# Kernel optimization log

Measured on AMD Instinct MI355X. Metric: run time of the kernel, lower is better.

## Reference

```python
import jax, jax.numpy as jnp
import numpy as np

N = 100000      # nodes
E = 1600000     # edges
IN_C = 128
HID = 64
OUT_C = 40
LAYERS = 8
ALPHA = 0.1
THETA = 0.5
BN_EPS = 1e-5


def setup_inputs() -> dict:
    key = jax.random.key(0)
    ks = jax.random.split(key, 8)
    x = jax.random.normal(ks[0], (N, IN_C), jnp.float32)
    edge_index = jax.random.randint(ks[1], (2, E), 0, N, dtype=jnp.int64)
    W0 = jax.random.normal(ks[2], (IN_C, HID), jnp.float32) / np.sqrt(IN_C).astype(np.float32)
    b0 = jnp.zeros((HID,), jnp.float32)
    convW = jax.random.normal(ks[3], (LAYERS, HID, HID), jnp.float32) / np.sqrt(HID).astype(np.float32)
    bn_gamma = jnp.ones((LAYERS, HID), jnp.float32)
    bn_beta = jnp.zeros((LAYERS, HID), jnp.float32)
    W_out = jax.random.normal(ks[4], (HID, OUT_C), jnp.float32) / np.sqrt(HID).astype(np.float32)
    b_out = jnp.zeros((OUT_C,), jnp.float32)
    return dict(x=x, edge_index=edge_index, W0=W0, b0=b0, convW=convW,
                bn_gamma=bn_gamma, bn_beta=bn_beta, W_out=W_out, b_out=b_out)


def _gcn_norm(edge_index, n):
    # gcn_norm with improved=False, add_self_loops=True (pyg default)
    loop = jnp.arange(n, dtype=edge_index.dtype)
    row = jnp.concatenate([edge_index[0], loop])
    col = jnp.concatenate([edge_index[1], loop])
    deg = jnp.zeros((n,), jnp.float32).at[col].add(1.0)  # deg >= 1 (self loops)
    dinv = jax.lax.rsqrt(deg)
    w = dinv[row] * dinv[col]
    return row, col, w


def reference(x, edge_index, W0, b0, convW, bn_gamma, bn_beta, W_out, b_out):
    n = x.shape[0]
    row, col, w = _gcn_norm(edge_index, n)
    # dropout in eval mode -> identity
    h = jax.nn.relu(x @ W0 + b0)
    h0 = h
    for i in range(LAYERS):
        beta = float(np.log(THETA / (i + 1) + 1.0))  # GCN2Conv beta for layer i+1
        # adj_t @ h: adj_t = transpose of normalized adjacency -> out[col] += w * h[row]
        agg = jnp.zeros_like(h).at[col].add(w[:, None] * h[row])
        s = (1.0 - ALPHA) * agg + ALPHA * h0              # initial residual
        s = (1.0 - beta) * s + beta * (s @ convW[i])      # identity mapping (shared_weights)
        mu = s.mean(axis=0)
        var = s.var(axis=0)                               # batchnorm (batch stats, biased var)
        s = (s - mu) * jax.lax.rsqrt(var + BN_EPS) * bn_gamma[i] + bn_beta[i]
        h = jax.nn.relu(s)
    return h @ W_out + b_out
```

## Files before the change

kernel.cpp:

```cpp
#include <hip/hip_runtime.h>
#include <math.h>

#define NTHREADS 256
#define IN_C 128
#define HID 64
#define OUT_C 40
#define N_LAYERS 8
#define ALPHA 0.1f
#define BN_EPS 1e-5f
#define BKT_SHIFT 9

typedef float f32x4 __attribute__((ext_vector_type(4)));
typedef _Float16 f16;
typedef _Float16 f16x4 __attribute__((ext_vector_type(4)));
typedef _Float16 f16x8 __attribute__((ext_vector_type(8)));

__device__ __forceinline__ f32x4 ld4(const float* p) { return *(const f32x4*)p; }

__device__ __forceinline__ f32x4 ldh4(const f16* p) {
  f16x4 v = *(const f16x4*)p;
  return __builtin_convertvector(v, f32x4);
}

__device__ __forceinline__ f32x4 bnrelu(f32x4 v, f32x4 k1, f32x4 k2) {
  f32x4 r = v * k1 + k2;
  r.x = fmaxf(r.x, 0.f); r.y = fmaxf(r.y, 0.f);
  r.z = fmaxf(r.z, 0.f); r.w = fmaxf(r.w, 0.f);
  return r;
}

__device__ __forceinline__ f32x4 xreduce(f32x4 v) {
  v.x += __shfl_xor(v.x, 16); v.y += __shfl_xor(v.y, 16);
  v.z += __shfl_xor(v.z, 16); v.w += __shfl_xor(v.w, 16);
  v.x += __shfl_xor(v.x, 32); v.y += __shfl_xor(v.y, 32);
  v.z += __shfl_xor(v.z, 32); v.w += __shfl_xor(v.w, 32);
  return v;
}


__global__ void k_zero(int* __restrict__ cnt, float* __restrict__ sumP,
                       float* __restrict__ sumsqP, f16* __restrict__ svpad,
                       int n) {
  int i = blockIdx.x * NTHREADS + threadIdx.x;
  if (i < n) cnt[i] = 0;
  if (i < N_LAYERS * 1024) { sumP[i] = 0.f; sumsqP[i] = 0.f; }
  if (i < 256) {
    f16x4 z = {(f16)0.f, (f16)0.f, (f16)0.f, (f16)0.f};
    ((f16x4*)svpad)[i] = z;
  }
}

__global__ void k_hist(const int* __restrict__ col, int* __restrict__ cnt, int E) {
  int e = blockIdx.x * NTHREADS + threadIdx.x;
  if (e < E) atomicAdd(&cnt[col[e]], 1);
}

__global__ void k_scan1(const int* __restrict__ cnt, int* __restrict__ offs,
                        int* __restrict__ partials, float* __restrict__ dinv,
                        int n) {
  __shared__ int sh[NTHREADS];
  int t = threadIdx.x, i = blockIdx.x * NTHREADS + t;
  int v = (i < n) ? cnt[i] : 0;
  if (i < n) dinv[i] = rsqrtf((float)v + 1.0f);
  sh[t] = v;
  __syncthreads();
  int run = v;
  for (int d = 1; d < NTHREADS; d <<= 1) {
    int add = (t >= d) ? sh[t - d] : 0;
    __syncthreads();
    run += add;
    sh[t] = run;
    __syncthreads();
  }
  if (i < n) offs[i] = run - v;
  if (t == NTHREADS - 1) partials[blockIdx.x] = run;
}

__global__ void k_scan2(int* __restrict__ partials, int nb) {
  __shared__ int sh[512];
  int t = threadIdx.x;
  int v = (t < nb) ? partials[t] : 0;
  sh[t] = v;
  __syncthreads();
  int run = v;
  for (int d = 1; d < 512; d <<= 1) {
    int add = (t >= d) ? sh[t - d] : 0;
    __syncthreads();
    run += add;
    sh[t] = run;
    __syncthreads();
  }
  if (t < nb) partials[t] = run - v;
}

__global__ void k_scan3(int* __restrict__ offs, int* __restrict__ cur,
                        const int* __restrict__ partials,
                        int* __restrict__ bcur, int n, int E) {
  int i = blockIdx.x * NTHREADS + threadIdx.x;
  if (i < n) {
    int v = offs[i] + partials[i >> 8];
    offs[i] = v;
    cur[i] = v;
    if ((i & ((1 << BKT_SHIFT) - 1)) == 0) bcur[i >> BKT_SHIFT] = v;
  }
  if (i == 0) offs[n] = E;
}

__global__ __launch_bounds__(NTHREADS) void k_bucketA(
    const int* __restrict__ row, const int* __restrict__ col,
    int* __restrict__ bcur, long long* __restrict__ tmp, int E, int nb) {
  __shared__ int lhist[512];
  __shared__ int lbase[512];
  int t = threadIdx.x;
  for (int i = t; i < nb; i += NTHREADS) lhist[i] = 0;
  __syncthreads();
  int start = blockIdx.x * 4096;
  int end = min(E, start + 4096);
  for (int e = start + t; e < end; e += NTHREADS)
    atomicAdd(&lhist[col[e] >> BKT_SHIFT], 1);
  __syncthreads();
  for (int i = t; i < nb; i += NTHREADS) {
    int c = lhist[i];
    lbase[i] = c ? atomicAdd(&bcur[i], c) : 0;
    lhist[i] = 0;
  }
  __syncthreads();
  for (int e = start + t; e < end; e += NTHREADS) {
    int cl = col[e];
    int b = cl >> BKT_SHIFT;
    int slot = atomicAdd(&lhist[b], 1);
    tmp[lbase[b] + slot] = ((long long)cl << 32) | (unsigned int)row[e];
  }
}

__global__ __launch_bounds__(NTHREADS) void k_bucketB(
    const long long* __restrict__ tmp, const int* __restrict__ offs,
    int* __restrict__ cur, int* __restrict__ ew, int n) {
  int b = blockIdx.x;
  int lo = b << BKT_SHIFT;
  int hi = min(n, lo + (1 << BKT_SHIFT));
  int s = offs[lo], e2 = offs[hi];
  for (int j = s + threadIdx.x; j < e2; j += NTHREADS) {
    long long r = tmp[j];
    int cl = (int)(r >> 32);
    int rw = (int)(r & 0xffffffffLL);
    int pos = atomicAdd(&cur[cl], 1);
    ew[pos] = rw;
  }
}

__global__ void k_gemm0(
    const float* __restrict__ x, const float* __restrict__ W0,
    const float* __restrict__ b0, const float* __restrict__ dinv,
    f16* __restrict__ h016, f16* __restrict__ hp, int n) {
  int t = threadIdx.x;
  int lane = t & 63, wid = t >> 6;
  int lm = lane & 15, lk = lane >> 4;
  f16x8 bf[4][4];
  float bv[4];
#pragma unroll
  for (int nt = 0; nt < 4; nt++) {
    int c = nt * 16 + lm;
    bv[nt] = b0[c];
#pragma unroll
    for (int ks = 0; ks < 4; ks++) {
#pragma unroll
      for (int i = 0; i < 8; i++) {
        bf[nt][ks][i] = (f16)W0[(ks * 32 + lk * 8 + i) * HID + c];
      }
    }
  }
  int nblk = (n + 15) >> 4;
  for (int blk = blockIdx.x * 4 + wid; blk < nblk; blk += gridDim.x * 4) {
    int r0 = blk * 16;
    int rA = min(r0 + lm, n - 1);
    const float* xr = x + (size_t)rA * IN_C + lk * 8;
    f16x8 af[4];
#pragma unroll
    for (int ks = 0; ks < 4; ks++) {
      f32x4 lo = ld4(xr + ks * 32);
      f32x4 hi = ld4(xr + ks * 32 + 4);
      f16x4 l16 = __builtin_convertvector(lo, f16x4);
      f16x4 h16 = __builtin_convertvector(hi, f16x4);
#pragma unroll
      for (int i = 0; i < 4; i++) { af[ks][i] = l16[i]; af[ks][4 + i] = h16[i]; }
    }
    float dv[4];
#pragma unroll
    for (int reg = 0; reg < 4; reg++)
      dv[reg] = dinv[min(r0 + lk * 4 + reg, n - 1)];
#pragma unroll
    for (int nt = 0; nt < 4; nt++) {
      f32x4 z = {0.f, 0.f, 0.f, 0.f};
      z = __builtin_amdgcn_mfma_f32_16x16x32_f16(af[0], bf[nt][0], z, 0, 0, 0);
      z = __builtin_amdgcn_mfma_f32_16x16x32_f16(af[1], bf[nt][1], z, 0, 0, 0);
      z = __builtin_amdgcn_mfma_f32_16x16x32_f16(af[2], bf[nt][2], z, 0, 0, 0);
      z = __builtin_amdgcn_mfma_f32_16x16x32_f16(af[3], bf[nt][3], z, 0, 0, 0);
#pragma unroll
      for (int reg = 0; reg < 4; reg++) {
        int r = r0 + lk * 4 + reg;
        if (r < n) {
          float v = fmaxf(z[reg] + bv[nt], 0.f);
          h016[(size_t)r * HID + nt * 16 + lm] = (f16)v;
          hp[(size_t)r * HID + nt * 16 + lm] = (f16)(dv[reg] * v);
        }
      }
    }
  }
}

__global__ void k_gather(
    const f16* __restrict__ hp, const f16* __restrict__ h0,
    const float* __restrict__ dinv, const int* __restrict__ offs,
    const int* __restrict__ ew, f16* __restrict__ sv, int n) {
  int t = threadIdx.x;
  int lane = t & 63;
  int eg = lane >> 4, li = lane & 15, c4 = li << 2;
  int i = blockIdx.x * 16 + (t >> 6) * 4 + eg;
  if (i >= n) return;
  int jb = offs[i], je = offs[i + 1];
  float di = dinv[i];
  f16x4 hs16 = *(const f16x4*)(hp + (size_t)i * HID + c4);
  f16x4 h016v = *(const f16x4*)(h0 + (size_t)i * HID + c4);
  f32x4 acc = {0.f, 0.f, 0.f, 0.f};
  int j = jb;
  for (; j + 8 <= je; j += 8) {
    int q0 = ew[j + 0];
    int q1 = ew[j + 1];
    int q2 = ew[j + 2];
    int q3 = ew[j + 3];
    int q4 = ew[j + 4];
    int q5 = ew[j + 5];
    int q6 = ew[j + 6];
    int q7 = ew[j + 7];
    f16x4 u0 = *(const f16x4*)(hp + (size_t)q0 * HID + c4);
    f16x4 u1 = *(const f16x4*)(hp + (size_t)q1 * HID + c4);
    f16x4 u2 = *(const f16x4*)(hp + (size_t)q2 * HID + c4);
    f16x4 u3 = *(const f16x4*)(hp + (size_t)q3 * HID + c4);
    f16x4 u4 = *(const f16x4*)(hp + (size_t)q4 * HID + c4);
    f16x4 u5 = *(const f16x4*)(hp + (size_t)q5 * HID + c4);
    f16x4 u6 = *(const f16x4*)(hp + (size_t)q6 * HID + c4);
    f16x4 u7 = *(const f16x4*)(hp + (size_t)q7 * HID + c4);
    acc += __builtin_convertvector(u0, f32x4);
    acc += __builtin_convertvector(u1, f32x4);
    acc += __builtin_convertvector(u2, f32x4);
    acc += __builtin_convertvector(u3, f32x4);
    acc += __builtin_convertvector(u4, f32x4);
    acc += __builtin_convertvector(u5, f32x4);
    acc += __builtin_convertvector(u6, f32x4);
    acc += __builtin_convertvector(u7, f32x4);
  }
  for (; j < je; j++) {
    acc += ldh4(hp + (size_t)ew[j] * HID + c4);
  }
  f32x4 hs = __builtin_convertvector(hs16, f32x4);
  f32x4 h0v = __builtin_convertvector(h016v, f32x4);
  f32x4 sval = (1.f - ALPHA) * (di * (acc + hs)) + ALPHA * h0v;
  *(f16x4*)(sv + (size_t)i * HID + c4) = __builtin_convertvector(sval, f16x4);
}

__global__ __launch_bounds__(NTHREADS) void k_conv(
    const f16* __restrict__ sv, const float* __restrict__ Wl,
    f16* __restrict__ sout, float* __restrict__ sumL,
    float* __restrict__ sumsqL, float beta, int n) {
  __shared__ __align__(16) float Wsh[HID * HID];
  __shared__ f32x4 red4[2][4][16];
  int t = threadIdx.x;
  for (int m = t; m < HID * HID / 4; m += NTHREADS) {
    f32x4 wv = ((const f32x4*)Wl)[m];
    wv *= beta;
    int base = m * 4;
    int k = base >> 6, c0 = base & 63;
    if (k >= c0 && k < c0 + 4) wv[k - c0] += (1.f - beta);
    ((f32x4*)Wsh)[m] = wv;
  }
  __syncthreads();
  int lane = t & 63, wid = t >> 6;
  int lm = lane & 15, lk = lane >> 4;
  f16x8 bf[4][2];
#pragma unroll
  for (int nt = 0; nt < 4; nt++) {
#pragma unroll
    for (int ks = 0; ks < 2; ks++) {
      int c = nt * 16 + lm;
#pragma unroll
      for (int i = 0; i < 8; i++) {
        int k = ks * 32 + lk * 8 + i;
        bf[nt][ks][i] = (f16)Wsh[k * HID + c];
      }
    }
  }
  float ssum[4] = {0.f, 0.f, 0.f, 0.f}, ssq[4] = {0.f, 0.f, 0.f, 0.f};
  int nblk = (n + 15) >> 4;
  for (int blk = blockIdx.x * 4 + wid; blk < nblk; blk += gridDim.x * 4) {
    int r0 = blk * 16;
    const f16* ap = sv + (size_t)(r0 + lm) * HID + lk * 8;
    f16x8 a0 = *(const f16x8*)(ap);
    f16x8 a1 = *(const f16x8*)(ap + 32);
#pragma unroll
    for (int nt = 0; nt < 4; nt++) {
      f32x4 z = {0.f, 0.f, 0.f, 0.f};
      z = __builtin_amdgcn_mfma_f32_16x16x32_f16(a0, bf[nt][0], z, 0, 0, 0);
      z = __builtin_amdgcn_mfma_f32_16x16x32_f16(a1, bf[nt][1], z, 0, 0, 0);
#pragma unroll
      for (int reg = 0; reg < 4; reg++) {
        int r = r0 + lk * 4 + reg;
        if (r < n) {
          float v = z[reg];
          sout[(size_t)r * HID + nt * 16 + lm] = (f16)v;
          ssum[nt] += v;
          ssq[nt] += v * v;
        }
      }
    }
  }
  f32x4 sumv = {ssum[0], ssum[1], ssum[2], ssum[3]};
  f32x4 sqv = {ssq[0], ssq[1], ssq[2], ssq[3]};
  sumv = xreduce(sumv);
  sqv = xreduce(sqv);
  if (lk == 0) { red4[0][wid][lm] = sumv; red4[1][wid][lm] = sqv; }
  __syncthreads();
  if (t < 16) {
    f32x4 a = red4[0][0][t] + red4[0][1][t] + red4[0][2][t] + red4[0][3][t];
    f32x4 b = red4[1][0][t] + red4[1][1][t] + red4[1][2][t] + red4[1][3][t];
    int js = (blockIdx.x & 15) * 64;
    atomicAdd(&sumL[js + 0 * 16 + t], a.x);
    atomicAdd(&sumL[js + 1 * 16 + t], a.y);
    atomicAdd(&sumL[js + 2 * 16 + t], a.z);
    atomicAdd(&sumL[js + 3 * 16 + t], a.w);
    atomicAdd(&sumsqL[js + 0 * 16 + t], b.x);
    atomicAdd(&sumsqL[js + 1 * 16 + t], b.y);
    atomicAdd(&sumsqL[js + 2 * 16 + t], b.z);
    atomicAdd(&sumsqL[js + 3 * 16 + t], b.w);
  }
}

__device__ __forceinline__ void stats_to_lds(
    const float* __restrict__ sumL, const float* __restrict__ sumsqL,
    const float* __restrict__ gamma_l, const float* __restrict__ beta_l,
    float* ms, int t, int n) {
  if (t < 64) {
    float s = 0.f, sq = 0.f;
#pragma unroll
    for (int j = 0; j < 16; j++) {
      s += sumL[j * 64 + t];
      sq += sumsqL[j * 64 + t];
    }
    float mu = s / (float)n;
    float var = sq / (float)n - mu * mu;
    float iv = rsqrtf(var + BN_EPS);
    float k1 = iv * gamma_l[t];
    ms[t] = k1;
    ms[64 + t] = beta_l[t] - mu * k1;
  }
  __syncthreads();
}

__global__ __launch_bounds__(NTHREADS) void k_bnrelu(
    const f16* __restrict__ s, const float* __restrict__ sumL,
    const float* __restrict__ sumsqL, const float* __restrict__ gamma_l,
    const float* __restrict__ beta_l, const float* __restrict__ dinv,
    f16* __restrict__ hp, int n) {
  __shared__ __align__(16) float ms[128];
  int t = threadIdx.x;
  stats_to_lds(sumL, sumsqL, gamma_l, beta_l, ms, t, n);
  int idx = blockIdx.x * NTHREADS + t;
  if (idx < n * (HID / 4)) {
    int c4 = idx & 15;
    int row = idx >> 4;
    f32x4 v = ldh4(s + (size_t)idx * 4);
    f32x4 k1 = *(const f32x4*)(ms + c4 * 4);
    f32x4 k2 = *(const f32x4*)(ms + 64 + c4 * 4);
    v = bnrelu(v, k1, k2);
    float di = dinv[row];
    v = di * v;
    ((f16x4*)hp)[idx] = __builtin_convertvector(v, f16x4);
  }
}

__global__ __launch_bounds__(NTHREADS) void k_out(
    const f16* __restrict__ s, const float* __restrict__ sumL,
    const float* __restrict__ sumsqL, const float* __restrict__ gamma_l,
    const float* __restrict__ beta_l, const float* __restrict__ Wout,
    const float* __restrict__ bout, float* __restrict__ out, int n) {
  __shared__ float Ws[HID * OUT_C];
  __shared__ float bs[OUT_C];
  __shared__ __align__(16) float ms[128];
  int t = threadIdx.x;
  for (int m = t; m < HID * OUT_C; m += NTHREADS) Ws[m] = Wout[m];
  if (t < OUT_C) bs[t] = bout[t];
  stats_to_lds(sumL, sumsqL, gamma_l, beta_l, ms, t, n);
  int idx = blockIdx.x * NTHREADS + t;
  if (idx < n * OUT_C) {
    int row = idx / OUT_C;
    int c = idx - row * OUT_C;
    float acc = bs[c];
    const f16* sr = s + (size_t)row * HID;
    for (int kk = 0; kk < HID / 4; kk++) {
      f32x4 a = ldh4(sr + kk * 4);
      f32x4 k1 = *(const f32x4*)(ms + kk * 4);
      f32x4 k2 = *(const f32x4*)(ms + 64 + kk * 4);
      a = bnrelu(a, k1, k2);
      int k = kk * 4;
      acc += a.x * Ws[(k + 0) * OUT_C + c] + a.y * Ws[(k + 1) * OUT_C + c] +
             a.z * Ws[(k + 2) * OUT_C + c] + a.w * Ws[(k + 3) * OUT_C + c];
    }
    out[idx] = acc;
  }
}


extern "C" void kernel_launch(void* const* d_in, const int* in_sizes, int n_in,
                              void* d_out, int out_size, void* d_ws, size_t ws_size,
                              hipStream_t stream) {
  const float* x = (const float*)d_in[0];
  const int* ei = (const int*)d_in[1];
  const float* W0 = (const float*)d_in[2];
  const float* b0 = (const float*)d_in[3];
  const float* convW = (const float*)d_in[4];
  const float* bn_gamma = (const float*)d_in[5];
  const float* bn_beta = (const float*)d_in[6];
  const float* W_out = (const float*)d_in[7];
  const float* b_out = (const float*)d_in[8];
  float* out = (float*)d_out;

  int n = in_sizes[0] / IN_C;
  int E = in_sizes[1] / 2;
  const int* row = ei;
  const int* col = ei + E;
  int NB = (n + (1 << BKT_SHIFT) - 1) >> BKT_SHIFT;

  char* w = (char*)d_ws;
  auto alloc = [&](size_t bytes) {
    char* p = w;
    w += (bytes + 255) & ~(size_t)255;
    return p;
  };
  float* dinv    = (float*)alloc((size_t)n * 4);
  int*   cnt     = (int*)alloc((size_t)n * 4);
  int*   offs    = (int*)alloc((size_t)(n + 1) * 4);
  int*   cur     = (int*)alloc((size_t)n * 4);
  int*   partials= (int*)alloc(512 * 4);
  int*   bcur    = (int*)alloc(512 * 4);
  int*   ew      = (int*)alloc((size_t)E * 4);
  long long* tmp = (long long*)alloc((size_t)E * 8);
  f16*   h016    = (f16*)alloc((size_t)n * HID * 2);
  f16*   hp      = (f16*)alloc((size_t)n * HID * 2);
  f16*   sv      = (f16*)alloc((size_t)(n + 16) * HID * 2);
  f16*   sb      = (f16*)alloc((size_t)n * HID * 2);
  float* sumP    = (float*)alloc((size_t)N_LAYERS * 1024 * 4);
  float* sumsqP  = (float*)alloc((size_t)N_LAYERS * 1024 * 4);

  int gN = (n + NTHREADS - 1) / NTHREADS;
  int gE = (E + NTHREADS - 1) / NTHREADS;
  int gA = (E + 4095) / 4096;
  int gRow = (n + 15) / 16;
  int gConv = (gRow + 3) / 4;
  int gV = (n * (HID / 4) + NTHREADS - 1) / NTHREADS;

  k_zero<<<gN, NTHREADS, 0, stream>>>(cnt, sumP, sumsqP,
                                      sv + (size_t)n * HID, n);
  k_hist<<<gE, NTHREADS, 0, stream>>>(col, cnt, E);
  k_scan1<<<gN, NTHREADS, 0, stream>>>(cnt, offs, partials, dinv, n);
  k_scan2<<<1, 512, 0, stream>>>(partials, gN);
  k_scan3<<<gN, NTHREADS, 0, stream>>>(offs, cur, partials, bcur, n, E);
  k_bucketA<<<gA, NTHREADS, 0, stream>>>(row, col, bcur, tmp, E, NB);
  k_bucketB<<<NB, NTHREADS, 0, stream>>>(tmp, offs, cur, ew, n);

  k_gemm0<<<512, NTHREADS, 0, stream>>>(x, W0, b0, dinv, h016, hp, n);

  for (int l = 0; l < N_LAYERS; l++) {
    float beta = logf(0.5f / (float)(l + 1) + 1.0f);
    if (l > 0) {
      k_bnrelu<<<gV, NTHREADS, 0, stream>>>(
          sb, sumP + (size_t)(l - 1) * 1024, sumsqP + (size_t)(l - 1) * 1024,
          bn_gamma + (l - 1) * HID, bn_beta + (l - 1) * HID, dinv, hp, n);
    }
    k_gather<<<gRow, NTHREADS, 0, stream>>>(hp, h016, dinv, offs, ew, sv, n);
    k_conv<<<gConv, NTHREADS, 0, stream>>>(sv, convW + (size_t)l * HID * HID,
                                           sb, sumP + (size_t)l * 1024,
                                           sumsqP + (size_t)l * 1024, beta, n);
  }

  k_out<<<((size_t)n * OUT_C + NTHREADS - 1) / NTHREADS, NTHREADS, 0, stream>>>(
      sb, sumP + (size_t)7 * 1024, sumsqP + (size_t)7 * 1024,
      bn_gamma + 7 * HID, bn_beta + 7 * HID, W_out, b_out, out, n);
}
```

Baseline: 772.4 us.

## Build CSR via bucket histogram and in-block local scan, dropping global per-node histogram

Replaces the per-node global atomic histogram and three-kernel scan with a shared-memory bucket histogram, a single-block bucket scan, and per-bucket local counting and scanning inside bucketB. That kernel now computes node offsets, degree-based dinv and scatter positions with shared-memory atomics instead of global ones. The aim is to cut global atomic traffic and kernel launches in the preprocessing stage. k_bscan uses 256 threads, so it assumes at most 256 buckets (n up to about 131k), and bucketB reads tmp twice.

Result: faster. 693.1 us (-10.3%).

```diff
diff --git a/kernel.cpp b/kernel.cpp
--- a/kernel.cpp
+++ b/kernel.cpp
@@ -38,72 +38,58 @@
 }
 
 
-__global__ void k_zero(int* __restrict__ cnt, float* __restrict__ sumP,
-                       float* __restrict__ sumsqP, f16* __restrict__ svpad,
-                       int n) {
+__global__ void k_zero(float* __restrict__ sumP, float* __restrict__ sumsqP,
+                       f16* __restrict__ svpad, int* __restrict__ bcnt) {
   int i = blockIdx.x * NTHREADS + threadIdx.x;
-  if (i < n) cnt[i] = 0;
   if (i < N_LAYERS * 1024) { sumP[i] = 0.f; sumsqP[i] = 0.f; }
   if (i < 256) {
     f16x4 z = {(f16)0.f, (f16)0.f, (f16)0.f, (f16)0.f};
     ((f16x4*)svpad)[i] = z;
   }
-}
-
-__global__ void k_hist(const int* __restrict__ col, int* __restrict__ cnt, int E) {
-  int e = blockIdx.x * NTHREADS + threadIdx.x;
-  if (e < E) atomicAdd(&cnt[col[e]], 1);
-}
-
-__global__ void k_scan1(const int* __restrict__ cnt, int* __restrict__ offs,
-                        int* __restrict__ partials, float* __restrict__ dinv,
-                        int n) {
-  __shared__ int sh[NTHREADS];
-  int t = threadIdx.x, i = blockIdx.x * NTHREADS + t;
-  int v = (i < n) ? cnt[i] : 0;
-  if (i < n) dinv[i] = rsqrtf((float)v + 1.0f);
+  if (blockIdx.x == 0 && threadIdx.x < 256) bcnt[threadIdx.x] = 0;
+}
+
+__global__ __launch_bounds__(NTHREADS) void k_bhist(
+    const int* __restrict__ col, int* __restrict__ bcnt, int E, int nb) {
+  __shared__ int lhist[512];
+  int t = threadIdx.x;
+  for (int i = t; i < nb; i += NTHREADS) lhist[i] = 0;
+  __syncthreads();
+  int start = blockIdx.x * 4096;
+  int end = min(E, start + 4096);
+  for (int e = start + t; e < end; e += NTHREADS)
+    atomicAdd(&lhist[col[e] >> BKT_SHIFT], 1);
+  __syncthreads();
+  for (int i = t; i < nb; i += NTHREADS) {
+    int c = lhist[i];
+    if (c) atomicAdd(&bcnt[i], c);
+  }
+}
+
+__global__ void k_bscan(const int* __restrict__ bcnt, int* __restrict__ bbase,
+                        int* __restrict__ bcur, int* __restrict__ offs,
+                        int nb, int n, int E) {
+  __shared__ int sh[256];
+  int t = threadIdx.x;
+  int v = (t < nb) ? bcnt[t] : 0;
   sh[t] = v;
   __syncthreads();
   int run = v;
-  for (int d = 1; d < NTHREADS; d <<= 1) {
+  for (int d = 1; d < 256; d <<= 1) {
     int add = (t >= d) ? sh[t - d] : 0;
     __syncthreads();
     run += add;
     sh[t] = run;
     __syncthreads();
   }
-  if (i < n) offs[i] = run - v;
-  if (t == NTHREADS - 1) partials[blockIdx.x] = run;
-}
-
-__global__ void k_scan2(int* __restrict__ partials, int nb) {
-  __shared__ int sh[512];
-  int t = threadIdx.x;
-  int v = (t < nb) ? partials[t] : 0;
-  sh[t] = v;
-  __syncthreads();
-  int run = v;
-  for (int d = 1; d < 512; d <<= 1) {
-    int add = (t >= d) ? sh[t - d] : 0;
-    __syncthreads();
-    run += add;
-    sh[t] = run;
-    __syncthreads();
-  }
-  if (t < nb) partials[t] = run - v;
-}
-
-__global__ void k_scan3(int* __restrict__ offs, int* __restrict__ cur,
-                        const int* __restrict__ partials,
-                        int* __restrict__ bcur, int n, int E) {
-  int i = blockIdx.x * NTHREADS + threadIdx.x;
-  if (i < n) {
-    int v = offs[i] + partials[i >> 8];
-    offs[i] = v;
-    cur[i] = v;
-    if ((i & ((1 << BKT_SHIFT) - 1)) == 0) bcur[i >> BKT_SHIFT] = v;
-  }
-  if (i == 0) offs[n] = E;
+  if (t < nb) {
+    bbase[t] = run - v;
+    bcur[t] = run - v;
+  }
+  if (t == 0) {
+    bbase[nb] = E;
+    offs[n] = E;
+  }
 }
 
 __global__ __launch_bounds__(NTHREADS) void k_bucketA(
@@ -133,19 +119,43 @@
   }
 }
 
-__global__ __launch_bounds__(NTHREADS) void k_bucketB(
-    const long long* __restrict__ tmp, const int* __restrict__ offs,
-    int* __restrict__ cur, int* __restrict__ ew, int n) {
+__global__ __launch_bounds__(512) void k_bucketB(
+    const long long* __restrict__ tmp, const int* __restrict__ bbase,
+    int* __restrict__ offs, float* __restrict__ dinv,
+    int* __restrict__ ew, int n) {
+  __shared__ int lcnt[512];
+  __shared__ int lcur[512];
   int b = blockIdx.x;
+  int t = threadIdx.x;
   int lo = b << BKT_SHIFT;
-  int hi = min(n, lo + (1 << BKT_SHIFT));
-  int s = offs[lo], e2 = offs[hi];
-  for (int j = s + threadIdx.x; j < e2; j += NTHREADS) {
+  int s = bbase[b], e2 = bbase[b + 1];
+  lcnt[t] = 0;
+  __syncthreads();
+  for (int j = s + t; j < e2; j += 512)
+    atomicAdd(&lcnt[(int)(tmp[j] >> 32) - lo], 1);
+  __syncthreads();
+  int v = lcnt[t];
+  int run = v;
+  for (int d = 1; d < 512; d <<= 1) {
+    int add = (t >= d) ? lcnt[t - d] : 0;
+    __syncthreads();
+    run += add;
+    lcnt[t] = run;
+    __syncthreads();
+  }
+  int node = lo + t;
+  int myoff = s + run - v;
+  if (node < n) {
+    offs[node] = myoff;
+    dinv[node] = rsqrtf((float)v + 1.0f);
+  }
+  lcur[t] = myoff;
+  __syncthreads();
+  for (int j = s + t; j < e2; j += 512) {
     long long r = tmp[j];
     int cl = (int)(r >> 32);
-    int rw = (int)(r & 0xffffffffLL);
-    int pos = atomicAdd(&cur[cl], 1);
-    ew[pos] = rw;
+    int pos = atomicAdd(&lcur[cl - lo], 1);
+    ew[pos] = (int)(r & 0xffffffffLL);
   }
 }
 
@@ -437,10 +447,9 @@
     return p;
   };
   float* dinv    = (float*)alloc((size_t)n * 4);
-  int*   cnt     = (int*)alloc((size_t)n * 4);
   int*   offs    = (int*)alloc((size_t)(n + 1) * 4);
-  int*   cur     = (int*)alloc((size_t)n * 4);
-  int*   partials= (int*)alloc(512 * 4);
+  int*   bcnt    = (int*)alloc(512 * 4);
+  int*   bbase   = (int*)alloc(512 * 4);
   int*   bcur    = (int*)alloc(512 * 4);
   int*   ew      = (int*)alloc((size_t)E * 4);
   long long* tmp = (long long*)alloc((size_t)E * 8);
@@ -451,21 +460,16 @@
   float* sumP    = (float*)alloc((size_t)N_LAYERS * 1024 * 4);
   float* sumsqP  = (float*)alloc((size_t)N_LAYERS * 1024 * 4);
 
-  int gN = (n + NTHREADS - 1) / NTHREADS;
-  int gE = (E + NTHREADS - 1) / NTHREADS;
-  int gA = (E + 4095) / 4096;
+  int gE4 = (E + 4095) / 4096;
   int gRow = (n + 15) / 16;
   int gConv = (gRow + 3) / 4;
   int gV = (n * (HID / 4) + NTHREADS - 1) / NTHREADS;
 
-  k_zero<<<gN, NTHREADS, 0, stream>>>(cnt, sumP, sumsqP,
-                                      sv + (size_t)n * HID, n);
-  k_hist<<<gE, NTHREADS, 0, stream>>>(col, cnt, E);
-  k_scan1<<<gN, NTHREADS, 0, stream>>>(cnt, offs, partials, dinv, n);
-  k_scan2<<<1, 512, 0, stream>>>(partials, gN);
-  k_scan3<<<gN, NTHREADS, 0, stream>>>(offs, cur, partials, bcur, n, E);
-  k_bucketA<<<gA, NTHREADS, 0, stream>>>(row, col, bcur, tmp, E, NB);
-  k_bucketB<<<NB, NTHREADS, 0, stream>>>(tmp, offs, cur, ew, n);
+  k_zero<<<33, NTHREADS, 0, stream>>>(sumP, sumsqP, sv + (size_t)n * HID, bcnt);
+  k_bhist<<<gE4, NTHREADS, 0, stream>>>(col, bcnt, E, NB);
+  k_bscan<<<1, 256, 0, stream>>>(bcnt, bbase, bcur, offs, NB, n, E);
+  k_bucketA<<<gE4, NTHREADS, 0, stream>>>(row, col, bcur, tmp, E, NB);
+  k_bucketB<<<NB, 512, 0, stream>>>(tmp, bbase, offs, dinv, ew, n);
 
   k_gemm0<<<512, NTHREADS, 0, stream>>>(x, W0, b0, dinv, h016, hp, n);
 
```
